# Kernel optimization log

Measured on AMD Instinct MI355X. Metric: run time of the kernel, lower is better.

The kernel has to match this reference:

```python
import jax, jax.numpy as jnp
import numpy as np

NUM_NODES = 100000
EMB_DIM = 64
NUM_LAYERS = 3
DROPOUT_P = 0.1
NUM_EDGES = 1200000


def setup_inputs() -> dict:
    key = jax.random.key(0)
    k1, k2 = jax.random.split(key)
    # Xavier-uniform init for the embedding table (as in the torch module)
    limit = (6.0 / (NUM_NODES + EMB_DIM)) ** 0.5
    emb_weight = jax.random.uniform(k1, (NUM_NODES, EMB_DIM), jnp.float32, -limit, limit)
    edge_index = jax.random.randint(k2, (2, NUM_EDGES), 0, NUM_NODES, dtype=jnp.int32)
    return {"emb_weight": emb_weight, "edge_index": edge_index}


def _lightgcn(x, edge_index):
    # Standard LightGCN propagation: x_{l+1} = A_hat x_l with symmetric norm,
    # output = mean over layer embeddings 0..L.
    src, dst = edge_index[0], edge_index[1]
    ones = jnp.ones((edge_index.shape[1],), dtype=x.dtype)
    deg = jax.ops.segment_sum(ones, dst, num_segments=NUM_NODES)
    deg_inv_sqrt = jnp.where(deg > 0, jax.lax.rsqrt(jnp.maximum(deg, 1.0)), 0.0)
    norm = deg_inv_sqrt[src] * deg_inv_sqrt[dst]  # [E]
    out = x
    acc = x
    for _ in range(NUM_LAYERS):
        msg = out[src] * norm[:, None]                       # gather [E, D]
        out = jax.ops.segment_sum(msg, dst, num_segments=NUM_NODES)  # scatter-add [N, D]
        acc = acc + out
    return acc / (NUM_LAYERS + 1)


def _dropout(x, p, key):
    keep = jax.random.bernoulli(key, 1.0 - p, x.shape)
    return jnp.where(keep, x / (1.0 - p), jnp.zeros((), x.dtype))


def reference(emb_weight, edge_index):
    out = _lightgcn(emb_weight, edge_index)
    # Dropout in train mode, fixed key for reproducibility
    return _dropout(out, DROPOUT_P, jax.random.key(42))
```

## Files before the change

### kernel.cpp

```cpp
#include <hip/hip_runtime.h>
#include <math.h>

#define N_NODES 100000
#define EMB 64
#define N_EDGES 1200000
#define N_ELEM (N_NODES * EMB)
#define SCAN_CHUNK 1024
#define SCAN_NBLK ((N_NODES + SCAN_CHUNK - 1) / SCAN_CHUNK)

__device__ __forceinline__ unsigned rotl32(unsigned v, int r) {
    return (v << r) | (v >> (32 - r));
}

__device__ __forceinline__ void threefry2x32(unsigned k0, unsigned k1,
                                             unsigned c0, unsigned c1,
                                             unsigned& o0, unsigned& o1) {
    const unsigned ks0 = k0;
    const unsigned ks1 = k1;
    const unsigned ks2 = k0 ^ k1 ^ 0x1BD11BDAu;
    unsigned x0 = c0 + ks0;
    unsigned x1 = c1 + ks1;
#define TF_RND(r) { x0 += x1; x1 = rotl32(x1, r); x1 ^= x0; }
    TF_RND(13) TF_RND(15) TF_RND(26) TF_RND(6)
    x0 += ks1; x1 += ks2 + 1u;
    TF_RND(17) TF_RND(29) TF_RND(16) TF_RND(24)
    x0 += ks2; x1 += ks0 + 2u;
    TF_RND(13) TF_RND(15) TF_RND(26) TF_RND(6)
    x0 += ks0; x1 += ks1 + 3u;
    TF_RND(17) TF_RND(29) TF_RND(16) TF_RND(24)
    x0 += ks1; x1 += ks2 + 4u;
    TF_RND(13) TF_RND(15) TF_RND(26) TF_RND(6)
    x0 += ks2; x1 += ks0 + 5u;
#undef TF_RND
    o0 = x0;
    o1 = x1;
}

__device__ __forceinline__ bool drop_keep(unsigned i) {
    unsigned o0, o1;
    threefry2x32(0u, 42u, 0u, i, o0, o1);
    unsigned bits = o0 ^ o1;
    float u = __uint_as_float((bits >> 9) | 0x3f800000u) - 1.0f;
    return u < 0.9f;
}

__global__ void k_hist(const int* __restrict__ dst, int* __restrict__ cnt) {
    int e = blockIdx.x * blockDim.x + threadIdx.x;
    if (e < N_EDGES) atomicAdd(&cnt[dst[e]], 1);
}

__global__ void k_scan1(const int* __restrict__ cnt, int* __restrict__ local,
                        int* __restrict__ bsum, float* __restrict__ dis) {
    __shared__ int wsum[16];
    const int tid = threadIdx.x;
    const int lane = tid & 63;
    const int wid = tid >> 6;
    int i = blockIdx.x * SCAN_CHUNK + tid;
    int v = (i < N_NODES) ? cnt[i] : 0;
    if (i < N_NODES) dis[i] = (v > 0) ? rsqrtf((float)v) : 0.0f;
    int x = v;
#pragma unroll
    for (int off = 1; off < 64; off <<= 1) {
        int t = __shfl_up(x, off, 64);
        if (lane >= off) x += t;
    }
    if (lane == 63) wsum[wid] = x;
    __syncthreads();
    if (wid == 0 && lane < 16) {
        int w = wsum[lane];
#pragma unroll
        for (int off = 1; off < 16; off <<= 1) {
            int t = __shfl_up(w, off, 64);
            if (lane >= off) w += t;
        }
        wsum[lane] = w;
    }
    __syncthreads();
    int wexc = (wid == 0) ? 0 : wsum[wid - 1];
    if (i < N_NODES) local[i] = (x + wexc) - v;
    if (tid == 0) bsum[blockIdx.x] = wsum[15];
}

__global__ void k_scan2(const int* __restrict__ bsum, int* __restrict__ bofs) {
    __shared__ int sh[128];
    int t = threadIdx.x;
    int v = (t < SCAN_NBLK) ? bsum[t] : 0;
    sh[t] = v;
    __syncthreads();
    for (int off = 1; off < 128; off <<= 1) {
        int add = (t >= off) ? sh[t - off] : 0;
        __syncthreads();
        sh[t] += add;
        __syncthreads();
    }
    if (t < SCAN_NBLK) bofs[t] = sh[t] - v;
}

__global__ void k_scan3(int* __restrict__ cursor_local, const int* __restrict__ bofs,
                        int* __restrict__ rowptr) {
    int i = blockIdx.x * SCAN_CHUNK + threadIdx.x;
    if (i < N_NODES) {
        int r = cursor_local[i] + bofs[blockIdx.x];
        rowptr[i] = r;
        cursor_local[i] = r;
    }
    if (i == 0) rowptr[N_NODES] = N_EDGES;
}

__global__ void k_scatter(const int* __restrict__ src, const int* __restrict__ dst,
                          const float* __restrict__ dis, int* __restrict__ cursor,
                          int2* __restrict__ edges) {
    int e = blockIdx.x * blockDim.x + threadIdx.x;
    if (e >= N_EDGES) return;
    int s = src[e];
    int d = dst[e];
    int pos = atomicAdd(&cursor[d], 1);
    edges[pos] = make_int2(s, __float_as_int(dis[s] * dis[d]));
}

template <int MODE>
__global__ void k_agg(const int* __restrict__ rowptr, const int2* __restrict__ edges,
                      const float* __restrict__ x, float* __restrict__ y,
                      float* __restrict__ acc) {
    int wv = (blockIdx.x * blockDim.x + threadIdx.x) >> 6;
    if (wv >= N_NODES) return;
    const int lane = threadIdx.x & 63;
    const int g = lane >> 4;
    const int l16 = lane & 15;
    const int begin = rowptr[wv];
    const int end = rowptr[wv + 1];
    float4 s = make_float4(0.f, 0.f, 0.f, 0.f);
    const float* xb = x + (size_t)(l16 << 2);
    for (int j = begin + g; j < end; j += 4) {
        int2 rec = edges[j];
        float nm = __int_as_float(rec.y);
        const float4 v = *reinterpret_cast<const float4*>(xb + (size_t)rec.x * EMB);
        s.x += v.x * nm; s.y += v.y * nm; s.z += v.z * nm; s.w += v.w * nm;
    }
    s.x += __shfl_xor(s.x, 16, 64); s.y += __shfl_xor(s.y, 16, 64);
    s.z += __shfl_xor(s.z, 16, 64); s.w += __shfl_xor(s.w, 16, 64);
    s.x += __shfl_xor(s.x, 32, 64); s.y += __shfl_xor(s.y, 32, 64);
    s.z += __shfl_xor(s.z, 32, 64); s.w += __shfl_xor(s.w, 32, 64);

    const size_t ridx = (size_t)wv * EMB + (l16 << 2);
    if (MODE == 0) {
        if (g == 0) *reinterpret_cast<float4*>(y + ridx) = s;
        if (g == 1) {
            float4 own = *reinterpret_cast<const float4*>(x + ridx);
            *reinterpret_cast<float4*>(acc + ridx) =
                make_float4(own.x + s.x, own.y + s.y, own.z + s.z, own.w + s.w);
        }
    } else if (MODE == 1) {
        if (g == 0) *reinterpret_cast<float4*>(y + ridx) = s;
        if (g == 1) {
            float4 a = *reinterpret_cast<const float4*>(acc + ridx);
            *reinterpret_cast<float4*>(acc + ridx) =
                make_float4(a.x + s.x, a.y + s.y, a.z + s.z, a.w + s.w);
        }
    } else {
        unsigned rowbase = (unsigned)((size_t)wv * EMB);
        bool k = drop_keep(rowbase + (unsigned)((l16 << 2) + g));
        unsigned long long mask = __ballot(k);
        if (g == 0) {
            float4 a = *reinterpret_cast<const float4*>(acc + ridx);
            float4 t = make_float4(a.x + s.x, a.y + s.y, a.z + s.z, a.w + s.w);
            const float sc = 0.25f / 0.9f;
            float4 o;
            o.x = ((mask >> (0 * 16 + l16)) & 1ull) ? t.x * sc : 0.f;
            o.y = ((mask >> (1 * 16 + l16)) & 1ull) ? t.y * sc : 0.f;
            o.z = ((mask >> (2 * 16 + l16)) & 1ull) ? t.z * sc : 0.f;
            o.w = ((mask >> (3 * 16 + l16)) & 1ull) ? t.w * sc : 0.f;
            *reinterpret_cast<float4*>(acc + ridx) = o;
        }
    }
}

extern "C" void kernel_launch(void* const* d_in, const int* in_sizes, int n_in,
                              void* d_out, int out_size, void* d_ws, size_t ws_size,
                              hipStream_t stream) {
    const float* emb = (const float*)d_in[0];
    const int* eidx = (const int*)d_in[1];
    const int* src = eidx;
    const int* dst = eidx + N_EDGES;
    float* acc = (float*)d_out;

    char* ws = (char*)d_ws;
    int*   cnt     = (int*)(ws + 0);
    int*   cursor  = (int*)(ws + 400000);
    int*   bsum    = (int*)(ws + 800000);
    int*   bofs    = (int*)(ws + 800400);
    int*   rowptr  = (int*)(ws + 800800);
    float* dis     = (float*)(ws + 1200808);
    int2*  edges   = (int2*)(ws + 1600808);
    float* bufA    = (float*)(ws + 11200816);
    float* bufB    = (float*)(ws + 36800816);

    const int BLK = 256;
    const int gE   = (N_EDGES + BLK - 1) / BLK;
    const int gAgg = (N_NODES * 64 + BLK - 1) / BLK;

    hipMemsetAsync(cnt, 0, N_NODES * sizeof(int), stream);
    k_hist<<<gE, BLK, 0, stream>>>(dst, cnt);
    k_scan1<<<SCAN_NBLK, SCAN_CHUNK, 0, stream>>>(cnt, cursor, bsum, dis);
    k_scan2<<<1, 128, 0, stream>>>(bsum, bofs);
    k_scan3<<<SCAN_NBLK, SCAN_CHUNK, 0, stream>>>(cursor, bofs, rowptr);
    k_scatter<<<gE, BLK, 0, stream>>>(src, dst, dis, cursor, edges);

    k_agg<0><<<gAgg, BLK, 0, stream>>>(rowptr, edges, emb,  bufA, acc);
    k_agg<1><<<gAgg, BLK, 0, stream>>>(rowptr, edges, bufA, bufB, acc);
    k_agg<2><<<gAgg, BLK, 0, stream>>>(rowptr, edges, bufB, nullptr, acc);
}
```

Baseline: 378.0 us.

## Fuse whole LightGCN pipeline into one cooperative persistent kernel with grid syncs

Replaces the nine-launch sequence (memset, histogram, three scan kernels, scatter, three aggregation passes) with a single cooperative kernel of 1024 blocks that separates the phases with grid-wide syncs and uses grid-stride loops. The aim is to remove per-launch overhead and inter-kernel gaps. The aggregation loop is also unrolled by two to keep more gathers in flight. In exchange, a persistent grid with fixed occupancy may hide latency less well in the gather-bound aggregation phases, and each grid sync has its own cost. The old multi-kernel path is kept as a fallback in case the cooperative launch fails.

```diff
diff --git a/kernel.cpp b/kernel.cpp
--- a/kernel.cpp
+++ b/kernel.cpp
@@ -1,12 +1,20 @@
 #include <hip/hip_runtime.h>
+#include <hip/hip_cooperative_groups.h>
 #include <math.h>
+
+namespace cg = cooperative_groups;
 
 #define N_NODES 100000
 #define EMB 64
 #define N_EDGES 1200000
 #define N_ELEM (N_NODES * EMB)
-#define SCAN_CHUNK 1024
-#define SCAN_NBLK ((N_NODES + SCAN_CHUNK - 1) / SCAN_CHUNK)
+#define GRID 1024
+#define TPB 256
+#define NTHREADS (GRID * TPB)
+#define NWAVES (NTHREADS / 64)
+#define SCAN_CHUNKS ((N_NODES + TPB - 1) / TPB)
+#define SCAN_CHUNK2 1024
+#define SCAN_NBLK2 ((N_NODES + SCAN_CHUNK2 - 1) / SCAN_CHUNK2)
 
 __device__ __forceinline__ unsigned rotl32(unsigned v, int r) {
     return (v << r) | (v >> (32 - r));
@@ -44,6 +52,169 @@
     return u < 0.9f;
 }
 
+template <int MODE>
+__device__ __forceinline__ void agg_body(const int* __restrict__ rowptr,
+                                         const int2* __restrict__ edges,
+                                         const float* __restrict__ x,
+                                         float* __restrict__ y,
+                                         float* __restrict__ acc,
+                                         int gwid, int nwaves, int lane) {
+    const int g = lane >> 4;
+    const int l16 = lane & 15;
+    const float* xb = x + (l16 << 2);
+    for (int wv = gwid; wv < N_NODES; wv += nwaves) {
+        const int begin = rowptr[wv];
+        const int end = rowptr[wv + 1];
+        float4 s = make_float4(0.f, 0.f, 0.f, 0.f);
+        int j = begin + g;
+        for (; j + 4 < end; j += 8) {
+            int2 r0 = edges[j];
+            int2 r1 = edges[j + 4];
+            float n0 = __int_as_float(r0.y);
+            float n1 = __int_as_float(r1.y);
+            const float4 v0 = *reinterpret_cast<const float4*>(xb + (size_t)r0.x * EMB);
+            const float4 v1 = *reinterpret_cast<const float4*>(xb + (size_t)r1.x * EMB);
+            s.x += v0.x * n0 + v1.x * n1;
+            s.y += v0.y * n0 + v1.y * n1;
+            s.z += v0.z * n0 + v1.z * n1;
+            s.w += v0.w * n0 + v1.w * n1;
+        }
+        if (j < end) {
+            int2 r0 = edges[j];
+            float n0 = __int_as_float(r0.y);
+            const float4 v0 = *reinterpret_cast<const float4*>(xb + (size_t)r0.x * EMB);
+            s.x += v0.x * n0; s.y += v0.y * n0; s.z += v0.z * n0; s.w += v0.w * n0;
+        }
+        s.x += __shfl_xor(s.x, 16, 64); s.y += __shfl_xor(s.y, 16, 64);
+        s.z += __shfl_xor(s.z, 16, 64); s.w += __shfl_xor(s.w, 16, 64);
+        s.x += __shfl_xor(s.x, 32, 64); s.y += __shfl_xor(s.y, 32, 64);
+        s.z += __shfl_xor(s.z, 32, 64); s.w += __shfl_xor(s.w, 32, 64);
+
+        const size_t ridx = (size_t)wv * EMB + (l16 << 2);
+        if (MODE == 0) {
+            if (g == 0) *reinterpret_cast<float4*>(y + ridx) = s;
+            if (g == 1) {
+                float4 own = *reinterpret_cast<const float4*>(x + ridx);
+                *reinterpret_cast<float4*>(acc + ridx) =
+                    make_float4(own.x + s.x, own.y + s.y, own.z + s.z, own.w + s.w);
+            }
+        } else if (MODE == 1) {
+            if (g == 0) *reinterpret_cast<float4*>(y + ridx) = s;
+            if (g == 1) {
+                float4 a = *reinterpret_cast<const float4*>(acc + ridx);
+                *reinterpret_cast<float4*>(acc + ridx) =
+                    make_float4(a.x + s.x, a.y + s.y, a.z + s.z, a.w + s.w);
+            }
+        } else {
+            unsigned rowbase = (unsigned)((size_t)wv * EMB);
+            bool k = drop_keep(rowbase + (unsigned)((l16 << 2) + g));
+            unsigned long long mask = __ballot(k);
+            if (g == 0) {
+                float4 a = *reinterpret_cast<const float4*>(acc + ridx);
+                float4 t = make_float4(a.x + s.x, a.y + s.y, a.z + s.z, a.w + s.w);
+                const float sc = 0.25f / 0.9f;
+                float4 o;
+                o.x = ((mask >> (0 * 16 + l16)) & 1ull) ? t.x * sc : 0.f;
+                o.y = ((mask >> (1 * 16 + l16)) & 1ull) ? t.y * sc : 0.f;
+                o.z = ((mask >> (2 * 16 + l16)) & 1ull) ? t.z * sc : 0.f;
+                o.w = ((mask >> (3 * 16 + l16)) & 1ull) ? t.w * sc : 0.f;
+                *reinterpret_cast<float4*>(acc + ridx) = o;
+            }
+        }
+    }
+}
+
+__global__ __launch_bounds__(TPB, 4)
+void kfused(const float* __restrict__ emb, const int* __restrict__ src,
+            const int* __restrict__ dst,
+            int* __restrict__ cnt, int* __restrict__ cursor,
+            int* __restrict__ bsum, int* __restrict__ bofs,
+            int* __restrict__ rowptr, float* __restrict__ dis,
+            int2* __restrict__ edges,
+            float* __restrict__ bufA, float* __restrict__ bufB,
+            float* __restrict__ acc) {
+    cg::grid_group grid = cg::this_grid();
+    const int tid = threadIdx.x;
+    const int bid = blockIdx.x;
+    const int gtid = bid * TPB + tid;
+    const int lane = tid & 63;
+    const int wid = tid >> 6;
+    const int gwid = gtid >> 6;
+
+    for (int i = gtid; i < N_NODES; i += NTHREADS) cnt[i] = 0;
+    grid.sync();
+
+    for (int e = gtid; e < N_EDGES; e += NTHREADS) atomicAdd(&cnt[dst[e]], 1);
+    grid.sync();
+
+    {
+        __shared__ int wsum[4];
+        for (int c = bid; c < SCAN_CHUNKS; c += GRID) {
+            int i = c * TPB + tid;
+            int v = (i < N_NODES) ? cnt[i] : 0;
+            if (i < N_NODES) dis[i] = (v > 0) ? rsqrtf((float)v) : 0.0f;
+            int x = v;
+#pragma unroll
+            for (int off = 1; off < 64; off <<= 1) {
+                int t = __shfl_up(x, off, 64);
+                if (lane >= off) x += t;
+            }
+            if (lane == 63) wsum[wid] = x;
+            __syncthreads();
+            int w0 = wsum[0], w1 = wsum[1], w2 = wsum[2], w3 = wsum[3];
+            int wexc = (wid > 0 ? w0 : 0) + (wid > 1 ? w1 : 0) + (wid > 2 ? w2 : 0);
+            if (i < N_NODES) cursor[i] = (x + wexc) - v;
+            if (tid == 0) bsum[c] = w0 + w1 + w2 + w3;
+            __syncthreads();
+        }
+    }
+    grid.sync();
+
+    if (bid == 0 && wid == 0) {
+        int carry = 0;
+        for (int base = 0; base < SCAN_CHUNKS; base += 64) {
+            int idx = base + lane;
+            int v = (idx < SCAN_CHUNKS) ? bsum[idx] : 0;
+            int x = v;
+#pragma unroll
+            for (int off = 1; off < 64; off <<= 1) {
+                int t = __shfl_up(x, off, 64);
+                if (lane >= off) x += t;
+            }
+            if (idx < SCAN_CHUNKS) bofs[idx] = carry + x - v;
+            carry += __shfl(x, 63, 64);
+        }
+    }
+    grid.sync();
+
+    for (int i = gtid; i < N_NODES; i += NTHREADS) {
+        int r = cursor[i] + bofs[i >> 8];
+        rowptr[i] = r;
+        cursor[i] = r;
+    }
+    if (gtid == 0) rowptr[N_NODES] = N_EDGES;
+    grid.sync();
+
+    for (int e = gtid; e < N_EDGES; e += NTHREADS) {
+        int s = src[e];
+        int d = dst[e];
+        int pos = atomicAdd(&cursor[d], 1);
+        edges[pos] = make_int2(s, __float_as_int(dis[s] * dis[d]));
+    }
+    grid.sync();
+
+    agg_body<0>(rowptr, edges, emb, bufA, acc, gwid, NWAVES, lane);
+    grid.sync();
+    agg_body<1>(rowptr, edges, bufA, bufB, acc, gwid, NWAVES, lane);
+    grid.sync();
+    agg_body<2>(rowptr, edges, bufB, nullptr, acc, gwid, NWAVES, lane);
+}
+
+__global__ void k_zero(int* __restrict__ p, int n) {
+    int i = blockIdx.x * blockDim.x + threadIdx.x;
+    if (i < n) p[i] = 0;
+}
+
 __global__ void k_hist(const int* __restrict__ dst, int* __restrict__ cnt) {
     int e = blockIdx.x * blockDim.x + threadIdx.x;
     if (e < N_EDGES) atomicAdd(&cnt[dst[e]], 1);
@@ -55,7 +226,7 @@
     const int tid = threadIdx.x;
     const int lane = tid & 63;
     const int wid = tid >> 6;
-    int i = blockIdx.x * SCAN_CHUNK + tid;
+    int i = blockIdx.x * SCAN_CHUNK2 + tid;
     int v = (i < N_NODES) ? cnt[i] : 0;
     if (i < N_NODES) dis[i] = (v > 0) ? rsqrtf((float)v) : 0.0f;
     int x = v;
@@ -84,7 +255,7 @@
 __global__ void k_scan2(const int* __restrict__ bsum, int* __restrict__ bofs) {
     __shared__ int sh[128];
     int t = threadIdx.x;
-    int v = (t < SCAN_NBLK) ? bsum[t] : 0;
+    int v = (t < SCAN_NBLK2) ? bsum[t] : 0;
     sh[t] = v;
     __syncthreads();
     for (int off = 1; off < 128; off <<= 1) {
@@ -93,12 +264,12 @@
         sh[t] += add;
         __syncthreads();
     }
-    if (t < SCAN_NBLK) bofs[t] = sh[t] - v;
+    if (t < SCAN_NBLK2) bofs[t] = sh[t] - v;
 }
 
 __global__ void k_scan3(int* __restrict__ cursor_local, const int* __restrict__ bofs,
                         int* __restrict__ rowptr) {
-    int i = blockIdx.x * SCAN_CHUNK + threadIdx.x;
+    int i = blockIdx.x * SCAN_CHUNK2 + threadIdx.x;
     if (i < N_NODES) {
         int r = cursor_local[i] + bofs[blockIdx.x];
         rowptr[i] = r;
@@ -122,57 +293,10 @@
 __global__ void k_agg(const int* __restrict__ rowptr, const int2* __restrict__ edges,
                       const float* __restrict__ x, float* __restrict__ y,
                       float* __restrict__ acc) {
-    int wv = (blockIdx.x * blockDim.x + threadIdx.x) >> 6;
-    if (wv >= N_NODES) return;
-    const int lane = threadIdx.x & 63;
-    const int g = lane >> 4;
-    const int l16 = lane & 15;
-    const int begin = rowptr[wv];
-    const int end = rowptr[wv + 1];
-    float4 s = make_float4(0.f, 0.f, 0.f, 0.f);
-    const float* xb = x + (size_t)(l16 << 2);
-    for (int j = begin + g; j < end; j += 4) {
-        int2 rec = edges[j];
-        float nm = __int_as_float(rec.y);
-        const float4 v = *reinterpret_cast<const float4*>(xb + (size_t)rec.x * EMB);
-        s.x += v.x * nm; s.y += v.y * nm; s.z += v.z * nm; s.w += v.w * nm;
-    }
-    s.x += __shfl_xor(s.x, 16, 64); s.y += __shfl_xor(s.y, 16, 64);
-    s.z += __shfl_xor(s.z, 16, 64); s.w += __shfl_xor(s.w, 16, 64);
-    s.x += __shfl_xor(s.x, 32, 64); s.y += __shfl_xor(s.y, 32, 64);
-    s.z += __shfl_xor(s.z, 32, 64); s.w += __shfl_xor(s.w, 32, 64);
-
-    const size_t ridx = (size_t)wv * EMB + (l16 << 2);
-    if (MODE == 0) {
-        if (g == 0) *reinterpret_cast<float4*>(y + ridx) = s;
-        if (g == 1) {
-            float4 own = *reinterpret_cast<const float4*>(x + ridx);
-            *reinterpret_cast<float4*>(acc + ridx) =
-                make_float4(own.x + s.x, own.y + s.y, own.z + s.z, own.w + s.w);
-        }
-    } else if (MODE == 1) {
-        if (g == 0) *reinterpret_cast<float4*>(y + ridx) = s;
-        if (g == 1) {
-            float4 a = *reinterpret_cast<const float4*>(acc + ridx);
-            *reinterpret_cast<float4*>(acc + ridx) =
-                make_float4(a.x + s.x, a.y + s.y, a.z + s.z, a.w + s.w);
-        }
-    } else {
-        unsigned rowbase = (unsigned)((size_t)wv * EMB);
-        bool k = drop_keep(rowbase + (unsigned)((l16 << 2) + g));
-        unsigned long long mask = __ballot(k);
-        if (g == 0) {
-            float4 a = *reinterpret_cast<const float4*>(acc + ridx);
-            float4 t = make_float4(a.x + s.x, a.y + s.y, a.z + s.z, a.w + s.w);
-            const float sc = 0.25f / 0.9f;
-            float4 o;
-            o.x = ((mask >> (0 * 16 + l16)) & 1ull) ? t.x * sc : 0.f;
-            o.y = ((mask >> (1 * 16 + l16)) & 1ull) ? t.y * sc : 0.f;
-            o.z = ((mask >> (2 * 16 + l16)) & 1ull) ? t.z * sc : 0.f;
-            o.w = ((mask >> (3 * 16 + l16)) & 1ull) ? t.w * sc : 0.f;
-            *reinterpret_cast<float4*>(acc + ridx) = o;
-        }
-    }
+    int gwid = (blockIdx.x * blockDim.x + threadIdx.x) >> 6;
+    int lane = threadIdx.x & 63;
+    if (gwid >= N_NODES) return;
+    agg_body<MODE>(rowptr, edges, x, y, acc, gwid, N_NODES, lane);
 }
 
 extern "C" void kernel_launch(void* const* d_in, const int* in_sizes, int n_in,
@@ -188,24 +312,37 @@
     int*   cnt     = (int*)(ws + 0);
     int*   cursor  = (int*)(ws + 400000);
     int*   bsum    = (int*)(ws + 800000);
-    int*   bofs    = (int*)(ws + 800400);
-    int*   rowptr  = (int*)(ws + 800800);
-    float* dis     = (float*)(ws + 1200808);
-    int2*  edges   = (int2*)(ws + 1600808);
-    float* bufA    = (float*)(ws + 11200816);
-    float* bufB    = (float*)(ws + 36800816);
+    int*   bofs    = (int*)(ws + 801564);
+    int*   rowptr  = (int*)(ws + 803128);
+    float* dis     = (float*)(ws + 1203132);
+    int2*  edges   = (int2*)(ws + 1603136);
+    float* bufA    = (float*)(ws + 11203136);
+    float* bufB    = (float*)(ws + 36803136);
+
+    const float* emb_a = emb;
+    const int* src_a = src;
+    const int* dst_a = dst;
+    void* args[] = {
+        (void*)&emb_a, (void*)&src_a, (void*)&dst_a,
+        (void*)&cnt, (void*)&cursor, (void*)&bsum, (void*)&bofs,
+        (void*)&rowptr, (void*)&dis, (void*)&edges,
+        (void*)&bufA, (void*)&bufB, (void*)&acc
+    };
+    hipError_t err = hipLaunchCooperativeKernel((void*)kfused, dim3(GRID), dim3(TPB),
+                                                args, 0, stream);
+    if (err == hipSuccess) return;
 
     const int BLK = 256;
     const int gE   = (N_EDGES + BLK - 1) / BLK;
+    const int gN   = (N_NODES + BLK - 1) / BLK;
     const int gAgg = (N_NODES * 64 + BLK - 1) / BLK;
 
-    hipMemsetAsync(cnt, 0, N_NODES * sizeof(int), stream);
+    k_zero<<<gN, BLK, 0, stream>>>(cnt, N_NODES);
     k_hist<<<gE, BLK, 0, stream>>>(dst, cnt);
-    k_scan1<<<SCAN_NBLK, SCAN_CHUNK, 0, stream>>>(cnt, cursor, bsum, dis);
+    k_scan1<<<SCAN_NBLK2, SCAN_CHUNK2, 0, stream>>>(cnt, cursor, bsum, dis);
     k_scan2<<<1, 128, 0, stream>>>(bsum, bofs);
-    k_scan3<<<SCAN_NBLK, SCAN_CHUNK, 0, stream>>>(cursor, bofs, rowptr);
+    k_scan3<<<SCAN_NBLK2, SCAN_CHUNK2, 0, stream>>>(cursor, bofs, rowptr);
     k_scatter<<<gE, BLK, 0, stream>>>(src, dst, dis, cursor, edges);
-
     k_agg<0><<<gAgg, BLK, 0, stream>>>(rowptr, edges, emb,  bufA, acc);
     k_agg<1><<<gAgg, BLK, 0, stream>>>(rowptr, edges, bufA, bufB, acc);
     k_agg<2><<<gAgg, BLK, 0, stream>>>(rowptr, edges, bufB, nullptr, acc);
```

Result: slower. 1.226 ms (+224.3%).

## Partition CSR scatter by destination range and map four nodes per wavefront

Applied to the files above, without the earlier changes.

The scatter kernel now uses a fixed grid in which each block handles one of eight destination-node partitions and skips edges outside it. This is meant to keep the atomic cursor updates and edge writes within a smaller address window for better cache locality, at the cost of every block reading the full dst array. The aggregation kernel now gives each 16-lane group its own node instead of splitting one node's edges across four groups. That removes the cross-group shuffle reduction and adds a 4-way unrolled gather for more memory-level parallelism, but it can increase load imbalance between nodes of different degree. In the final layer each lane now computes its own dropout bits with threefry instead of sharing them through a ballot, which means four RNG calls per lane.

```diff
diff --git a/kernel.cpp b/kernel.cpp
--- a/kernel.cpp
+++ b/kernel.cpp
@@ -7,6 +7,10 @@
 #define N_ELEM (N_NODES * EMB)
 #define SCAN_CHUNK 1024
 #define SCAN_NBLK ((N_NODES + SCAN_CHUNK - 1) / SCAN_CHUNK)
+#define NPART 8
+#define PART_SIZE (N_NODES / NPART)
+#define SC_GRID 1024
+#define SC_TPB 256
 
 __device__ __forceinline__ unsigned rotl32(unsigned v, int r) {
     return (v << r) | (v >> (32 - r));
@@ -110,68 +114,80 @@
 __global__ void k_scatter(const int* __restrict__ src, const int* __restrict__ dst,
                           const float* __restrict__ dis, int* __restrict__ cursor,
                           int2* __restrict__ edges) {
-    int e = blockIdx.x * blockDim.x + threadIdx.x;
-    if (e >= N_EDGES) return;
-    int s = src[e];
-    int d = dst[e];
-    int pos = atomicAdd(&cursor[d], 1);
-    edges[pos] = make_int2(s, __float_as_int(dis[s] * dis[d]));
+    const int p = blockIdx.x & (NPART - 1);
+    const int lo = p * PART_SIZE;
+    const int hi = lo + PART_SIZE;
+    const int stride = (SC_GRID / NPART) * SC_TPB;
+    int e = (blockIdx.x >> 3) * SC_TPB + threadIdx.x;
+    for (; e < N_EDGES; e += stride) {
+        int d = dst[e];
+        if (d >= lo && d < hi) {
+            int s = src[e];
+            int pos = atomicAdd(&cursor[d], 1);
+            edges[pos] = make_int2(s, __float_as_int(dis[s] * dis[d]));
+        }
+    }
 }
 
 template <int MODE>
 __global__ void k_agg(const int* __restrict__ rowptr, const int2* __restrict__ edges,
                       const float* __restrict__ x, float* __restrict__ y,
                       float* __restrict__ acc) {
-    int wv = (blockIdx.x * blockDim.x + threadIdx.x) >> 6;
-    if (wv >= N_NODES) return;
+    const int gwid = (blockIdx.x * blockDim.x + threadIdx.x) >> 6;
     const int lane = threadIdx.x & 63;
     const int g = lane >> 4;
     const int l16 = lane & 15;
-    const int begin = rowptr[wv];
-    const int end = rowptr[wv + 1];
+    const int n = (gwid << 2) + g;
+    if (n >= N_NODES) return;
+    const int begin = rowptr[n];
+    const int end = rowptr[n + 1];
+    const float* xb = x + (l16 << 2);
     float4 s = make_float4(0.f, 0.f, 0.f, 0.f);
-    const float* xb = x + (size_t)(l16 << 2);
-    for (int j = begin + g; j < end; j += 4) {
-        int2 rec = edges[j];
-        float nm = __int_as_float(rec.y);
-        const float4 v = *reinterpret_cast<const float4*>(xb + (size_t)rec.x * EMB);
-        s.x += v.x * nm; s.y += v.y * nm; s.z += v.z * nm; s.w += v.w * nm;
-    }
-    s.x += __shfl_xor(s.x, 16, 64); s.y += __shfl_xor(s.y, 16, 64);
-    s.z += __shfl_xor(s.z, 16, 64); s.w += __shfl_xor(s.w, 16, 64);
-    s.x += __shfl_xor(s.x, 32, 64); s.y += __shfl_xor(s.y, 32, 64);
-    s.z += __shfl_xor(s.z, 32, 64); s.w += __shfl_xor(s.w, 32, 64);
-
-    const size_t ridx = (size_t)wv * EMB + (l16 << 2);
+    int j = begin;
+    for (; j + 3 < end; j += 4) {
+        int2 r0 = edges[j];
+        int2 r1 = edges[j + 1];
+        int2 r2 = edges[j + 2];
+        int2 r3 = edges[j + 3];
+        const float4 v0 = *reinterpret_cast<const float4*>(xb + (size_t)r0.x * EMB);
+        const float4 v1 = *reinterpret_cast<const float4*>(xb + (size_t)r1.x * EMB);
+        const float4 v2 = *reinterpret_cast<const float4*>(xb + (size_t)r2.x * EMB);
+        const float4 v3 = *reinterpret_cast<const float4*>(xb + (size_t)r3.x * EMB);
+        float n0 = __int_as_float(r0.y), n1 = __int_as_float(r1.y);
+        float n2 = __int_as_float(r2.y), n3 = __int_as_float(r3.y);
+        s.x += v0.x * n0 + v1.x * n1 + v2.x * n2 + v3.x * n3;
+        s.y += v0.y * n0 + v1.y * n1 + v2.y * n2 + v3.y * n3;
+        s.z += v0.z * n0 + v1.z * n1 + v2.z * n2 + v3.z * n3;
+        s.w += v0.w * n0 + v1.w * n1 + v2.w * n2 + v3.w * n3;
+    }
+    for (; j < end; ++j) {
+        int2 r0 = edges[j];
+        float n0 = __int_as_float(r0.y);
+        const float4 v0 = *reinterpret_cast<const float4*>(xb + (size_t)r0.x * EMB);
+        s.x += v0.x * n0; s.y += v0.y * n0; s.z += v0.z * n0; s.w += v0.w * n0;
+    }
+    const size_t ridx = (size_t)n * EMB + (l16 << 2);
     if (MODE == 0) {
-        if (g == 0) *reinterpret_cast<float4*>(y + ridx) = s;
-        if (g == 1) {
-            float4 own = *reinterpret_cast<const float4*>(x + ridx);
-            *reinterpret_cast<float4*>(acc + ridx) =
-                make_float4(own.x + s.x, own.y + s.y, own.z + s.z, own.w + s.w);
-        }
+        *reinterpret_cast<float4*>(y + ridx) = s;
+        float4 own = *reinterpret_cast<const float4*>(x + ridx);
+        *reinterpret_cast<float4*>(acc + ridx) =
+            make_float4(own.x + s.x, own.y + s.y, own.z + s.z, own.w + s.w);
     } else if (MODE == 1) {
-        if (g == 0) *reinterpret_cast<float4*>(y + ridx) = s;
-        if (g == 1) {
-            float4 a = *reinterpret_cast<const float4*>(acc + ridx);
-            *reinterpret_cast<float4*>(acc + ridx) =
-                make_float4(a.x + s.x, a.y + s.y, a.z + s.z, a.w + s.w);
-        }
+        *reinterpret_cast<float4*>(y + ridx) = s;
+        float4 a = *reinterpret_cast<const float4*>(acc + ridx);
+        *reinterpret_cast<float4*>(acc + ridx) =
+            make_float4(a.x + s.x, a.y + s.y, a.z + s.z, a.w + s.w);
     } else {
-        unsigned rowbase = (unsigned)((size_t)wv * EMB);
-        bool k = drop_keep(rowbase + (unsigned)((l16 << 2) + g));
-        unsigned long long mask = __ballot(k);
-        if (g == 0) {
-            float4 a = *reinterpret_cast<const float4*>(acc + ridx);
-            float4 t = make_float4(a.x + s.x, a.y + s.y, a.z + s.z, a.w + s.w);
-            const float sc = 0.25f / 0.9f;
-            float4 o;
-            o.x = ((mask >> (0 * 16 + l16)) & 1ull) ? t.x * sc : 0.f;
-            o.y = ((mask >> (1 * 16 + l16)) & 1ull) ? t.y * sc : 0.f;
-            o.z = ((mask >> (2 * 16 + l16)) & 1ull) ? t.z * sc : 0.f;
-            o.w = ((mask >> (3 * 16 + l16)) & 1ull) ? t.w * sc : 0.f;
-            *reinterpret_cast<float4*>(acc + ridx) = o;
-        }
+        float4 a = *reinterpret_cast<const float4*>(acc + ridx);
+        float4 t = make_float4(a.x + s.x, a.y + s.y, a.z + s.z, a.w + s.w);
+        const float sc = 0.25f / 0.9f;
+        unsigned base = (unsigned)ridx;
+        float4 o;
+        o.x = drop_keep(base + 0u) ? t.x * sc : 0.f;
+        o.y = drop_keep(base + 1u) ? t.y * sc : 0.f;
+        o.z = drop_keep(base + 2u) ? t.z * sc : 0.f;
+        o.w = drop_keep(base + 3u) ? t.w * sc : 0.f;
+        *reinterpret_cast<float4*>(acc + ridx) = o;
     }
 }
 
@@ -197,14 +213,14 @@
 
     const int BLK = 256;
     const int gE   = (N_EDGES + BLK - 1) / BLK;
-    const int gAgg = (N_NODES * 64 + BLK - 1) / BLK;
+    const int gAgg = ((N_NODES + 3) / 4 * 64 + BLK - 1) / BLK;
 
     hipMemsetAsync(cnt, 0, N_NODES * sizeof(int), stream);
     k_hist<<<gE, BLK, 0, stream>>>(dst, cnt);
     k_scan1<<<SCAN_NBLK, SCAN_CHUNK, 0, stream>>>(cnt, cursor, bsum, dis);
     k_scan2<<<1, 128, 0, stream>>>(bsum, bofs);
     k_scan3<<<SCAN_NBLK, SCAN_CHUNK, 0, stream>>>(cursor, bofs, rowptr);
-    k_scatter<<<gE, BLK, 0, stream>>>(src, dst, dis, cursor, edges);
+    k_scatter<<<SC_GRID, SC_TPB, 0, stream>>>(src, dst, dis, cursor, edges);
 
     k_agg<0><<<gAgg, BLK, 0, stream>>>(rowptr, edges, emb,  bufA, acc);
     k_agg<1><<<gAgg, BLK, 0, stream>>>(rowptr, edges, bufA, bufB, acc);
```

New measurement: 368.4 us. 2.5% less time.
